# Optimization experiments

Hardware: AMD Instinct MI355X
Metric: run time of the kernel (lower is better)

## Reference

```python
import jax, jax.numpy as jnp
import numpy as np

B, S, D = 2048, 200, 128   # batch, n_steps, embedding dim per vector
H = 64                      # hidden_dim
MASK_SCALE = 1e10


def setup_inputs() -> dict:
    key = jax.random.key(0)
    ks = jax.random.split(key, 6)
    his = jax.random.normal(ks[0], (B, S, D), dtype=jnp.float32)
    target = jax.random.normal(ks[1], (B, 1, D), dtype=jnp.float32)
    # mask == 1.0 marks padded history positions (they get -1e10 added pre-softmax)
    mask = (jax.random.uniform(ks[2], (B, S)) < 0.3).astype(jnp.float32)
    W = jax.random.normal(ks[3], (3 * D, H), dtype=jnp.float32) * 0.1
    W_bias = jnp.full((H,), 0.1, dtype=jnp.float32)
    O = jax.random.normal(ks[4], (H, 1), dtype=jnp.float32) * 0.1
    O_bias = jnp.full((1,), 0.1, dtype=jnp.float32)
    return {"his": his, "target": target, "mask": mask,
            "W": W, "W_bias": W_bias, "O": O, "O_bias": O_bias}


def reference(his, target, mask, W, W_bias, O, O_bias):
    tgt = jnp.broadcast_to(target, his.shape)          # [B,S,D] tile over steps
    diff = his - tgt
    att_vec = jnp.concatenate([his, diff, tgt], axis=2)  # [B,S,3D]
    h = jax.nn.relu(jnp.einsum('bsf,fh->bsh', att_vec, W) + W_bias)  # [B,S,H]
    alpha = jnp.einsum('bsh,ho->bso', h, O) + O_bias   # [B,S,1]
    alpha = alpha[:, :, 0] - mask * MASK_SCALE         # [B,S]
    attn = jax.nn.softmax(alpha, axis=-1)              # [B,S]
    out = jnp.einsum('bs,bsd->bd', attn, his)          # weighted-sum pooling
    return out
```

## Files before the change

kernel.cpp:

```cpp
#include <hip/hip_runtime.h>

#define B_ 2048
#define S_ 200
#define D_ 128
#define H_ 64
#define MASK_SCALE 1e10f

typedef __attribute__((ext_vector_type(8))) short short8_t;
typedef __attribute__((ext_vector_type(4))) float f32x4;
typedef __attribute__((ext_vector_type(4))) unsigned short ushort4_t;

__device__ __forceinline__ unsigned short f2bf(float f) {
    unsigned u = __float_as_uint(f);
    unsigned r = (u + 0x7fffu + ((u >> 16) & 1u)) >> 16;
    return (unsigned short)r;
}
__device__ __forceinline__ float bf2f(unsigned short v) {
    return __uint_as_float(((unsigned)v) << 16);
}

__global__ __launch_bounds__(256) void prep_w(const float* __restrict__ W,
                                              unsigned short* __restrict__ wfrag) {
    int idx = blockIdx.x * 256 + threadIdx.x;
    int d = idx >> 6;
    int h = idx & 63;
    float w1 = W[d * H_ + h];
    float w2 = W[(D_ + d) * H_ + h];
    int kt = d >> 5, q = (d >> 3) & 3, j = d & 7;
    int nt = h >> 4, lm = h & 15;
    int lane = (q << 4) | lm;
    wfrag[((kt * 4 + nt) * 64 + lane) * 8 + j] = f2bf(w1 + w2);
}

__global__ __launch_bounds__(256, 3) void fused_kernel(const float* __restrict__ his,
                                                       const float* __restrict__ target,
                                                       const float* __restrict__ mask,
                                                       const float* __restrict__ W,
                                                       const float* __restrict__ W_bias,
                                                       const float* __restrict__ Ovec,
                                                       const unsigned short* __restrict__ wfrag,
                                                       float* __restrict__ out) {
    __shared__ unsigned short hisb[S_ * D_];
    __shared__ float alpha_s[208];
    __shared__ float red8[8];
    __shared__ float tp_s[H_];
    __shared__ float ov_s[H_];
    __shared__ float pool_s[3 * D_];

    const int b    = blockIdx.x;
    const int t    = threadIdx.x;
    const int lane = t & 63;
    const int wv   = t >> 6;
    const int lm   = lane & 15;
    const int q    = lane >> 4;

    float mk = (t < S_) ? mask[(size_t)b * S_ + t] : 0.f;

    short8_t bfrag[16];
    #pragma unroll
    for (int f = 0; f < 16; ++f)
        bfrag[f] = *(const short8_t*)(wfrag + ((size_t)(f * 64 + lane)) * 8);

    if (wv < 3) {
        const float4* hb4 = (const float4*)(his + (size_t)b * S_ * D_);
        const int tid3 = wv * 64 + lane;
        for (int i = tid3; i < S_ * D_ / 4; i += 192) {
            float4 x = hb4[i];
            ushort4_t v;
            v[0] = f2bf(x.x); v[1] = f2bf(x.y); v[2] = f2bf(x.z); v[3] = f2bf(x.w);
            *(ushort4_t*)(&hisb[i * 4]) = v;
        }
    } else {
        const float* tg = target + (size_t)b * D_;
        float acc = W_bias[lane];
        #pragma unroll 4
        for (int d = 0; d < D_; ++d) {
            float w2 = W[(D_ + d) * H_ + lane];
            float w3 = W[(2 * D_ + d) * H_ + lane];
            acc = fmaf(tg[d], w3 - w2, acc);
        }
        tp_s[lane] = acc;
        ov_s[lane] = Ovec[lane];
    }
    __syncthreads();

    for (int tile = wv; tile < 13; tile += 4) {
        int row0 = tile * 16;
        int ar = row0 + lm; if (ar > S_ - 1) ar = S_ - 1;
        const unsigned short* ap = &hisb[ar * D_ + q * 8];

        f32x4 acc[4];
        #pragma unroll
        for (int nt = 0; nt < 4; ++nt) acc[nt] = (f32x4){0.f, 0.f, 0.f, 0.f};

        #pragma unroll
        for (int kt = 0; kt < 4; ++kt) {
            short8_t a = *(const short8_t*)(ap + kt * 32);
            #pragma unroll
            for (int nt = 0; nt < 4; ++nt)
                acc[nt] = __builtin_amdgcn_mfma_f32_16x16x32_bf16(a, bfrag[kt * 4 + nt], acc[nt], 0, 0, 0);
        }

        float part[4];
        #pragma unroll
        for (int r = 0; r < 4; ++r) {
            float sum = 0.f;
            #pragma unroll
            for (int nt = 0; nt < 4; ++nt) {
                int h = nt * 16 + lm;
                float v = acc[nt][r] + tp_s[h];
                v = fmaxf(v, 0.f);
                sum = fmaf(v, ov_s[h], sum);
            }
            part[r] = sum;
        }
        #pragma unroll
        for (int off = 1; off < 16; off <<= 1) {
            #pragma unroll
            for (int r = 0; r < 4; ++r)
                part[r] += __shfl_xor(part[r], off);
        }
        if (lm == 0) {
            #pragma unroll
            for (int r = 0; r < 4; ++r)
                alpha_s[row0 + q * 4 + r] = part[r];
        }
    }
    __syncthreads();

    float a = (t < S_) ? alpha_s[t] - mk * MASK_SCALE : -INFINITY;
    float m = a;
    #pragma unroll
    for (int off = 1; off < 64; off <<= 1) m = fmaxf(m, __shfl_xor(m, off));
    if (lane == 0) red8[wv] = m;
    __syncthreads();
    m = fmaxf(fmaxf(red8[0], red8[1]), fmaxf(red8[2], red8[3]));
    float e = (t < S_) ? __expf(a - m) : 0.f;
    float ssum = e;
    #pragma unroll
    for (int off = 1; off < 64; off <<= 1) ssum += __shfl_xor(ssum, off);
    if (lane == 0) red8[4 + wv] = ssum;
    __syncthreads();
    float inv = 1.f / (red8[4] + red8[5] + red8[6] + red8[7]);
    __syncthreads();
    if (t < S_) alpha_s[t] = e * inv;
    __syncthreads();

    const int d4 = t & 31;
    const int sg = t >> 5;
    float acc0 = 0.f, acc1 = 0.f, acc2 = 0.f, acc3 = 0.f;
    for (int s = sg; s < S_; s += 8) {
        float w = alpha_s[s];
        ushort4_t v = *(const ushort4_t*)(&hisb[s * D_ + d4 * 4]);
        acc0 = fmaf(w, bf2f(v[0]), acc0);
        acc1 = fmaf(w, bf2f(v[1]), acc1);
        acc2 = fmaf(w, bf2f(v[2]), acc2);
        acc3 = fmaf(w, bf2f(v[3]), acc3);
    }
    acc0 += __shfl_xor(acc0, 32);
    acc1 += __shfl_xor(acc1, 32);
    acc2 += __shfl_xor(acc2, 32);
    acc3 += __shfl_xor(acc3, 32);
    if (wv && lane < 32) {
        float4 p; p.x = acc0; p.y = acc1; p.z = acc2; p.w = acc3;
        *(float4*)(&pool_s[(wv - 1) * D_ + d4 * 4]) = p;
    }
    __syncthreads();
    if (wv == 0 && lane < 32) {
        #pragma unroll
        for (int k = 0; k < 3; ++k) {
            const float4 p = *(const float4*)(&pool_s[k * D_ + d4 * 4]);
            acc0 += p.x; acc1 += p.y; acc2 += p.z; acc3 += p.w;
        }
        float4 o; o.x = acc0; o.y = acc1; o.z = acc2; o.w = acc3;
        *(float4*)(out + (size_t)b * D_ + d4 * 4) = o;
    }
}

extern "C" void kernel_launch(void* const* d_in, const int* in_sizes, int n_in,
                              void* d_out, int out_size, void* d_ws, size_t ws_size,
                              hipStream_t stream) {
    const float* his    = (const float*)d_in[0];
    const float* target = (const float*)d_in[1];
    const float* mask   = (const float*)d_in[2];
    const float* W      = (const float*)d_in[3];
    const float* W_bias = (const float*)d_in[4];
    const float* Ovec   = (const float*)d_in[5];
    float* out = (float*)d_out;

    unsigned short* wfrag = (unsigned short*)d_ws;

    prep_w<<<32, 256, 0, stream>>>(W, wfrag);
    fused_kernel<<<B_, 256, 0, stream>>>(his, target, mask, W, W_bias, Ovec, wfrag, out);
}
```

Measured before the change: 347.6 us.

## Move target projection to prep kernel, load history with all waves, swizzle LDS

The per-batch target projection (target·(W3−W2)+bias) moves out of the fused kernel into an extended prep kernel that writes it to workspace. This frees the fourth wave, so all 256 threads now stream the history tile to LDS with five independent float4 loads in flight per batch of the loop. The bf16 history in LDS is stored with an XOR swizzle on 16-byte chunks to cut bank conflicts for the MFMA row reads and the pooling reads. The cost is a larger prep launch and an extra global round trip for the projection.

```diff
diff --git a/kernel.cpp b/kernel.cpp
--- a/kernel.cpp
+++ b/kernel.cpp
@@ -19,26 +19,43 @@
     return __uint_as_float(((unsigned)v) << 16);
 }
 
-__global__ __launch_bounds__(256) void prep_w(const float* __restrict__ W,
-                                              unsigned short* __restrict__ wfrag) {
-    int idx = blockIdx.x * 256 + threadIdx.x;
-    int d = idx >> 6;
-    int h = idx & 63;
-    float w1 = W[d * H_ + h];
-    float w2 = W[(D_ + d) * H_ + h];
-    int kt = d >> 5, q = (d >> 3) & 3, j = d & 7;
-    int nt = h >> 4, lm = h & 15;
-    int lane = (q << 4) | lm;
-    wfrag[((kt * 4 + nt) * 64 + lane) * 8 + j] = f2bf(w1 + w2);
+__global__ __launch_bounds__(256) void prep(const float* __restrict__ W,
+                                            const float* __restrict__ W_bias,
+                                            const float* __restrict__ target,
+                                            unsigned short* __restrict__ wfrag,
+                                            float* __restrict__ tproj) {
+    const int blk = blockIdx.x;
+    const int t = threadIdx.x;
+    if (blk < 32) {
+        int idx = blk * 256 + t;
+        int d = idx >> 6;
+        int h = idx & 63;
+        float w1 = W[d * H_ + h];
+        float w2 = W[(D_ + d) * H_ + h];
+        int kt = d >> 5, q = (d >> 3) & 3, j = d & 7;
+        int nt = h >> 4, lm = h & 15;
+        int lane = (q << 4) | lm;
+        wfrag[((kt * 4 + nt) * 64 + lane) * 8 + j] = f2bf(w1 + w2);
+    } else {
+        int lane = t & 63, wv = t >> 6;
+        int bb = (blk - 32) * 4 + wv;
+        const float* tg = target + (size_t)bb * D_;
+        float acc = W_bias[lane];
+        #pragma unroll 4
+        for (int d = 0; d < D_; ++d) {
+            float w2 = W[(D_ + d) * H_ + lane];
+            float w3 = W[(2 * D_ + d) * H_ + lane];
+            acc = fmaf(tg[d], w3 - w2, acc);
+        }
+        tproj[bb * H_ + lane] = acc;
+    }
 }
 
 __global__ __launch_bounds__(256, 3) void fused_kernel(const float* __restrict__ his,
-                                                       const float* __restrict__ target,
                                                        const float* __restrict__ mask,
-                                                       const float* __restrict__ W,
-                                                       const float* __restrict__ W_bias,
+                                                       const unsigned short* __restrict__ wfrag,
+                                                       const float* __restrict__ tproj,
                                                        const float* __restrict__ Ovec,
-                                                       const unsigned short* __restrict__ wfrag,
                                                        float* __restrict__ out) {
     __shared__ unsigned short hisb[S_ * D_];
     __shared__ float alpha_s[208];
@@ -55,39 +72,40 @@
     const int q    = lane >> 4;
 
     float mk = (t < S_) ? mask[(size_t)b * S_ + t] : 0.f;
+    if (t < H_) {
+        tp_s[t] = tproj[b * H_ + t];
+        ov_s[t] = Ovec[t];
+    }
 
     short8_t bfrag[16];
     #pragma unroll
     for (int f = 0; f < 16; ++f)
         bfrag[f] = *(const short8_t*)(wfrag + ((size_t)(f * 64 + lane)) * 8);
 
-    if (wv < 3) {
-        const float4* hb4 = (const float4*)(his + (size_t)b * S_ * D_);
-        const int tid3 = wv * 64 + lane;
-        for (int i = tid3; i < S_ * D_ / 4; i += 192) {
-            float4 x = hb4[i];
+    const float4* hb4 = (const float4*)(his + (size_t)b * S_ * D_);
+    #pragma unroll
+    for (int g = 0; g < 5; ++g) {
+        float4 x[5];
+        #pragma unroll
+        for (int j = 0; j < 5; ++j)
+            x[j] = hb4[t + (g * 5 + j) * 256];
+        #pragma unroll
+        for (int j = 0; j < 5; ++j) {
+            int i  = t + (g * 5 + j) * 256;
+            int s  = i >> 5;
+            int d8 = i & 31;
+            int pc = (d8 >> 1) ^ (s & 15);
             ushort4_t v;
-            v[0] = f2bf(x.x); v[1] = f2bf(x.y); v[2] = f2bf(x.z); v[3] = f2bf(x.w);
-            *(ushort4_t*)(&hisb[i * 4]) = v;
-        }
-    } else {
-        const float* tg = target + (size_t)b * D_;
-        float acc = W_bias[lane];
-        #pragma unroll 4
-        for (int d = 0; d < D_; ++d) {
-            float w2 = W[(D_ + d) * H_ + lane];
-            float w3 = W[(2 * D_ + d) * H_ + lane];
-            acc = fmaf(tg[d], w3 - w2, acc);
-        }
-        tp_s[lane] = acc;
-        ov_s[lane] = Ovec[lane];
+            v[0] = f2bf(x[j].x); v[1] = f2bf(x[j].y);
+            v[2] = f2bf(x[j].z); v[3] = f2bf(x[j].w);
+            *(ushort4_t*)((char*)hisb + s * 256 + pc * 16 + (d8 & 1) * 8) = v;
+        }
     }
     __syncthreads();
 
     for (int tile = wv; tile < 13; tile += 4) {
         int row0 = tile * 16;
         int ar = row0 + lm; if (ar > S_ - 1) ar = S_ - 1;
-        const unsigned short* ap = &hisb[ar * D_ + q * 8];
 
         f32x4 acc[4];
         #pragma unroll
@@ -95,7 +113,8 @@
 
         #pragma unroll
         for (int kt = 0; kt < 4; ++kt) {
-            short8_t a = *(const short8_t*)(ap + kt * 32);
+            int c = (kt * 4 + q) ^ (ar & 15);
+            short8_t a = *(const short8_t*)((const char*)hisb + ar * 256 + c * 16);
             #pragma unroll
             for (int nt = 0; nt < 4; ++nt)
                 acc[nt] = __builtin_amdgcn_mfma_f32_16x16x32_bf16(a, bfrag[kt * 4 + nt], acc[nt], 0, 0, 0);
@@ -146,12 +165,14 @@
     if (t < S_) alpha_s[t] = e * inv;
     __syncthreads();
 
-    const int d4 = t & 31;
+    const int d8 = t & 31;
     const int sg = t >> 5;
     float acc0 = 0.f, acc1 = 0.f, acc2 = 0.f, acc3 = 0.f;
+    #pragma unroll 5
     for (int s = sg; s < S_; s += 8) {
         float w = alpha_s[s];
-        ushort4_t v = *(const ushort4_t*)(&hisb[s * D_ + d4 * 4]);
+        int pc = (d8 >> 1) ^ (s & 15);
+        ushort4_t v = *(const ushort4_t*)((const char*)hisb + s * 256 + pc * 16 + (d8 & 1) * 8);
         acc0 = fmaf(w, bf2f(v[0]), acc0);
         acc1 = fmaf(w, bf2f(v[1]), acc1);
         acc2 = fmaf(w, bf2f(v[2]), acc2);
@@ -163,17 +184,17 @@
     acc3 += __shfl_xor(acc3, 32);
     if (wv && lane < 32) {
         float4 p; p.x = acc0; p.y = acc1; p.z = acc2; p.w = acc3;
-        *(float4*)(&pool_s[(wv - 1) * D_ + d4 * 4]) = p;
+        *(float4*)(&pool_s[(wv - 1) * D_ + d8 * 4]) = p;
     }
     __syncthreads();
     if (wv == 0 && lane < 32) {
         #pragma unroll
         for (int k = 0; k < 3; ++k) {
-            const float4 p = *(const float4*)(&pool_s[k * D_ + d4 * 4]);
+            const float4 p = *(const float4*)(&pool_s[k * D_ + d8 * 4]);
             acc0 += p.x; acc1 += p.y; acc2 += p.z; acc3 += p.w;
         }
         float4 o; o.x = acc0; o.y = acc1; o.z = acc2; o.w = acc3;
-        *(float4*)(out + (size_t)b * D_ + d4 * 4) = o;
+        *(float4*)(out + (size_t)b * D_ + d8 * 4) = o;
     }
 }
 
@@ -188,8 +209,10 @@
     const float* Ovec   = (const float*)d_in[5];
     float* out = (float*)d_out;
 
-    unsigned short* wfrag = (unsigned short*)d_ws;
-
-    prep_w<<<32, 256, 0, stream>>>(W, wfrag);
-    fused_kernel<<<B_, 256, 0, stream>>>(his, target, mask, W, W_bias, Ovec, wfrag, out);
-}
+    char* ws = (char*)d_ws;
+    unsigned short* wfrag = (unsigned short*)ws;
+    float* tproj          = (float*)(ws + 16384);
+
+    prep<<<544, 256, 0, stream>>>(W, W_bias, target, wfrag, tproj);
+    fused_kernel<<<B_, 256, 0, stream>>>(his, mask, wfrag, tproj, Ovec, out);
+}
```

New measurement: 320.1 us. 1.09x faster.
